# Kernel optimization log

Hardware: AMD Instinct MI355X
Metric: run time of the kernel (lower is better)

## Reference

```python
import jax, jax.numpy as jnp
import numpy as np

R = 4           # max_displacement
P = 2 * R + 1   # search_range = 9
DILATIONS = [[1], [1, 2, 3, 5, 9, 16]]
STRIDES = [4, 1]  # 8 // encoder_output_stride for strides [2, 8]
EPS = 1e-9


def _l2norm(x):
    # torch: x / (x.norm(dim=1, keepdim=True) + 1e-9)
    return x / (jnp.linalg.norm(x, axis=1, keepdims=True) + EPS)


def _corr(x1, x2, dilation, stride):
    """SpatialCorrelationSampler(patch_size=9, stride=stride, padding=0,
    dilation_patch=dilation): out[b,u,v,i,j] = sum_c x1[b,c,i*s,j*s] *
    x2[b,c,i*s+(u-R)*d, j*s+(v-R)*d], zero outside bounds."""
    B, C, H, W = x1.shape
    pad = R * dilation
    x2p = jnp.pad(x2, ((0, 0), (0, 0), (pad, pad), (pad, pad)))
    x1s = x1[:, :, ::stride, ::stride]  # (B,C,Ho,Wo)
    Ho, Wo = x1s.shape[2], x1s.shape[3]
    # all 81 (u,v) patch-offset slice starts in the padded map
    uv = jnp.stack(jnp.meshgrid(jnp.arange(P), jnp.arange(P), indexing='ij'),
                   axis=-1).reshape(-1, 2) * dilation  # (81, 2)

    def step(carry, start):
        x2uv = jax.lax.dynamic_slice(x2p, (0, 0, start[0], start[1]), (B, C, H, W))
        x2uv = x2uv[:, :, ::stride, ::stride]
        return carry, jnp.sum(x1s * x2uv, axis=1)  # (B,Ho,Wo)

    _, cost = jax.lax.scan(step, None, uv)  # (81,B,Ho,Wo)
    cost = cost.reshape(P, P, B, Ho, Wo)
    return jnp.transpose(cost, (2, 0, 1, 3, 4))  # (B,P,P,Ho,Wo)


def setup_inputs() -> dict:
    key = jax.random.key(0)
    k0, k1, k2, k3 = jax.random.split(key, 4)
    return {
        'x1_0': jax.random.normal(k0, (4, 256, 192, 256), dtype=jnp.float32),
        'x1_1': jax.random.normal(k1, (4, 256, 48, 64), dtype=jnp.float32),
        'x2_0': jax.random.normal(k2, (4, 256, 192, 256), dtype=jnp.float32),
        'x2_1': jax.random.normal(k3, (4, 256, 48, 64), dtype=jnp.float32),
    }


def reference(x1_0, x1_1, x2_0, x2_1):
    xs1, xs2 = [x1_0, x1_1], [x2_0, x2_1]
    cost_list = []
    for x1, x2, dils, s in zip(xs1, xs2, DILATIONS, STRIDES):
        x1n = _l2norm(x1)
        x2n = _l2norm(x2)
        per_dil = [_corr(x1n, x2n, d, s) for d in dils]  # each (B,P,P,Ho,Wo)
        # num_groups=1: per-dilation volumes stack into dim 1
        cost_list.append(jnp.stack(per_dil, axis=1))  # (B,nd,P,P,Ho,Wo)
    return jnp.concatenate(cost_list, axis=1)  # (B,7,9,9,48,64)
```

## Files before the change

### kernel.cpp

```cpp
#include <hip/hip_runtime.h>
#include <stdint.h>

#define EPSN 1e-9f

typedef __fp16 f16x8 __attribute__((ext_vector_type(8)));
typedef float f32x4 __attribute__((ext_vector_type(4)));

#define LDS_FENCE()                                        \
  do {                                                     \
    asm volatile("s_waitcnt lgkmcnt(0)" ::: "memory");     \
    __builtin_amdgcn_sched_barrier(0);                     \
  } while (0)


__global__ __launch_bounds__(256) void norms1_kernel(
    const float* __restrict__ x1_1, const float* __restrict__ x2_1,
    float* __restrict__ ws) {
  int p = blockIdx.x * 256 + threadIdx.x;
  const float* src = (p < 12288) ? x1_1 : x2_1;
  int q = (p < 12288) ? p : p - 12288;
  long base = (long)(q / 3072) * 786432 + (q % 3072);
  float ss = 0.f;
#pragma unroll 8
  for (int c = 0; c < 256; ++c) { float v = src[base + (long)c * 3072]; ss += v * v; }
  ws[p] = 1.f / (sqrtf(ss) + EPSN);
}

__global__ __launch_bounds__(256) void xpose0_kernel(
    const float* __restrict__ x1, __fp16* __restrict__ x1h0) {
  int bx = blockIdx.x;
  int i = bx % 48, b = bx / 48;
  __fp16* dst = x1h0 + (long)(b * 48 + i) * 16384;
  __shared__ uint32_t lds[64 * 128];
  __shared__ float sred[4][64];
  int t = threadIdx.x;
  int j = t & 63, cg = t >> 6;
  const float* sp = x1 + (long)b * 12582912 + (long)(4 * i) * 256 + 4 * j;
  float vv[64];
  float ss = 0.f;
#pragma unroll
  for (int c8 = 0; c8 < 64; ++c8) {
    float v = sp[(long)(cg * 64 + c8) * 49152];
    vv[c8] = v;
    ss += v * v;
  }
  sred[cg][j] = ss;
  __syncthreads();
  float invv = 1.f / (sqrtf(sred[0][j] + sred[1][j] + sred[2][j] + sred[3][j]) + EPSN);
#pragma unroll
  for (int cb = 0; cb < 8; ++cb) {
    uint32_t pk[4];
#pragma unroll
    for (int e2 = 0; e2 < 4; ++e2) {
      int cl = cb * 8 + e2 * 2;
      __fp16 h0 = (__fp16)(vv[cl] * invv);
      __fp16 h1 = (__fp16)(vv[cl + 1] * invv);
      pk[e2] = (uint32_t)__builtin_bit_cast(uint16_t, h0) |
               ((uint32_t)__builtin_bit_cast(uint16_t, h1) << 16);
    }
    int byteoff = j * 512 + ((cg * 128 + cb * 16) ^ ((j & 7) << 4));
    *reinterpret_cast<uint4*>(reinterpret_cast<char*>(lds) + byteoff) =
        make_uint4(pk[0], pk[1], pk[2], pk[3]);
  }
  __syncthreads();
#pragma unroll
  for (int rep = 0; rep < 8; ++rep) {
    int idx = rep * 256 + t;
    int jj = idx >> 5, cb = idx & 31;
    int byteoff = jj * 512 + ((cb * 16) ^ ((jj & 7) << 4));
    uint4 val = *reinterpret_cast<const uint4*>(
        reinterpret_cast<const char*>(lds) + byteoff);
    *reinterpret_cast<uint4*>(reinterpret_cast<char*>(dst) + jj * 512 + cb * 16) = val;
  }
}

__global__ __launch_bounds__(256) void corr0f_kernel(
    const __fp16* __restrict__ x1h, const float* __restrict__ x2,
    float* __restrict__ out) {
  int bx = blockIdx.x;
  int L = (bx & 7) * 96 + (bx >> 3);
  int y = L % 192, b = L / 192;
  int tid = threadIdx.x;
  int w = tid >> 6, lane = tid & 63;
  int i_lo = (y - 1) / 4; if (i_lo < 0) i_lo = 0;
  int i_hi = (y + 4) / 4; if (i_hi > 47) i_hi = 47;
  int NI = i_hi - i_lo + 1;

  __shared__ float red[4][31][64];
  __shared__ float inv2s[264];

  float acc[3][9];
#pragma unroll
  for (int r = 0; r < 3; ++r)
#pragma unroll
    for (int v = 0; v < 9; ++v) acc[r][v] = 0.f;
  float sq0 = 0.f, sq1 = 0.f, sq2 = 0.f, sq3 = 0.f;

  const float* x2row = x2 + (long)b * 12582912 + (long)y * 256 + 4 * lane;
  int lm = (lane == 0) ? 0 : lane - 1;
  int lp = (lane == 63) ? 63 : lane + 1;
  const __fp16 *pc[3], *pl[3], *pr[3];
#pragma unroll
  for (int r = 0; r < 3; ++r) {
    int ir = i_lo + r; if (ir > 47) ir = 47;
    const __fp16* base = x1h + (long)(b * 48 + ir) * 16384;
    pc[r] = base + lane * 256;
    pl[r] = base + lm * 256;
    pr[r] = base + lp * 256;
  }

#pragma unroll 1
  for (int g = 0; g < 8; ++g) {
    int c0 = w * 64 + g * 8;
    float4 fv[8];
#pragma unroll
    for (int e = 0; e < 8; ++e)
      fv[e] = *reinterpret_cast<const float4*>(x2row + (long)(c0 + e) * 49152);
    f16x8 hc[3], hl[3], hr[3];
#pragma unroll
    for (int r = 0; r < 3; ++r) {
      hc[r] = __builtin_bit_cast(f16x8, *reinterpret_cast<const uint4*>(pc[r] + c0));
      hl[r] = __builtin_bit_cast(f16x8, *reinterpret_cast<const uint4*>(pl[r] + c0));
      hr[r] = __builtin_bit_cast(f16x8, *reinterpret_cast<const uint4*>(pr[r] + c0));
    }
#pragma unroll
    for (int e = 0; e < 8; ++e) {
      float4 f = fv[e];
      sq0 += f.x * f.x; sq1 += f.y * f.y; sq2 += f.z * f.z; sq3 += f.w * f.w;
#pragma unroll
      for (int r = 0; r < 3; ++r) {
        float xv  = (float)hc[r][e];
        float xrr = (float)hr[r][e];
        float xll = (float)hl[r][e];
        acc[r][0] += xrr * f.x; acc[r][1] += xrr * f.y;
        acc[r][2] += xrr * f.z; acc[r][3] += xrr * f.w;
        acc[r][4] += xv * f.x;  acc[r][5] += xv * f.y;
        acc[r][6] += xv * f.z;  acc[r][7] += xv * f.w;
        acc[r][8] += xll * f.x;
      }
    }
  }

#pragma unroll
  for (int r = 0; r < 3; ++r) {
    acc[r][0] = __shfl_up(acc[r][0], 1);
    acc[r][1] = __shfl_up(acc[r][1], 1);
    acc[r][2] = __shfl_up(acc[r][2], 1);
    acc[r][3] = __shfl_up(acc[r][3], 1);
    acc[r][8] = __shfl_down(acc[r][8], 1);
  }

#pragma unroll
  for (int r = 0; r < 3; ++r)
#pragma unroll
    for (int v = 0; v < 9; ++v) red[w][r * 9 + v][lane] = acc[r][v];
  red[w][27][lane] = sq0; red[w][28][lane] = sq1;
  red[w][29][lane] = sq2; red[w][30][lane] = sq3;
  __syncthreads();
  {
    int comp = tid & 3, jj = tid >> 2;
    float ss = red[0][27 + comp][jj] + red[1][27 + comp][jj] +
               red[2][27 + comp][jj] + red[3][27 + comp][jj];
    inv2s[4 + tid] = 1.f / (sqrtf(ss) + EPSN);
    if (tid < 4) { inv2s[tid] = 0.f; inv2s[260 + tid] = 0.f; }
  }
  __syncthreads();
  int lim = NI * 576;
  for (int idx = tid; idx < lim; idx += 256) {
    int r = idx / 576, rem = idx - r * 576;
    int v = rem >> 6, j = rem & 63;
    int i_r = i_lo + r;
    int u_r = y - 4 * i_r + 4;
    float s = red[0][r * 9 + v][j] + red[1][r * 9 + v][j] +
              red[2][r * 9 + v][j] + red[3][r * 9 + v][j];
    out[(long)b * 1741824 + (long)u_r * 27648 + (long)v * 3072 + i_r * 64 + j] =
        s * inv2s[4 * j + v];
  }
}

__global__ __launch_bounds__(256) void corr0_fb_kernel(
    const float* __restrict__ x1b, const float* __restrict__ x2,
    float* __restrict__ out) {
  int bx = blockIdx.x;
  int L = (bx & 7) * 96 + (bx >> 3);
  int y = L % 192, b = L / 192;
  int tid = threadIdx.x;
  int w = tid >> 6, lane = tid & 63;
  int i_lo = (y - 1) / 4; if (i_lo < 0) i_lo = 0;
  int i_hi = (y + 4) / 4; if (i_hi > 47) i_hi = 47;
  int NI = i_hi - i_lo + 1;
  __shared__ float red[4][34][64];
  __shared__ float inv2s[264];
  __shared__ float inv1s[3][64];
  float acc[3][9];
#pragma unroll
  for (int r = 0; r < 3; ++r)
#pragma unroll
    for (int v = 0; v < 9; ++v) acc[r][v] = 0.f;
  float sq0 = 0.f, sq1 = 0.f, sq2 = 0.f, sq3 = 0.f;
  float s1[3] = {0.f, 0.f, 0.f};
  const float* x2row = x2 + (long)b * 12582912 + (long)y * 256 + 4 * lane;
  const float* x1p[3];
#pragma unroll
  for (int r = 0; r < 3; ++r) {
    int ir = i_lo + r; if (ir > 47) ir = 47;
    x1p[r] = x1b + (long)b * 12582912 + (long)ir * 1024 + (long)lane * 4;
  }
#pragma unroll 4
  for (int cc = 0; cc < 64; ++cc) {
    int c = w * 64 + cc;
    long off2 = (long)c * 49152;
    long off1 = (long)c * 49152;
    float4 f = *reinterpret_cast<const float4*>(x2row + off2);
    sq0 += f.x * f.x; sq1 += f.y * f.y; sq2 += f.z * f.z; sq3 += f.w * f.w;
#pragma unroll
    for (int r = 0; r < 3; ++r) {
      float xv = x1p[r][off1];
      float xr = __shfl_down(xv, 1);
      float xl = __shfl_up(xv, 1);
      s1[r] += xv * xv;
      acc[r][0] += xr * f.x; acc[r][1] += xr * f.y;
      acc[r][2] += xr * f.z; acc[r][3] += xr * f.w;
      acc[r][4] += xv * f.x; acc[r][5] += xv * f.y;
      acc[r][6] += xv * f.z; acc[r][7] += xv * f.w;
      acc[r][8] += xl * f.x;
    }
  }
#pragma unroll
  for (int r = 0; r < 3; ++r) {
    red[w][r * 9 + 0][lane] = __shfl_up(acc[r][0], 1);
    red[w][r * 9 + 1][lane] = __shfl_up(acc[r][1], 1);
    red[w][r * 9 + 2][lane] = __shfl_up(acc[r][2], 1);
    red[w][r * 9 + 3][lane] = __shfl_up(acc[r][3], 1);
    red[w][r * 9 + 4][lane] = acc[r][4];
    red[w][r * 9 + 5][lane] = acc[r][5];
    red[w][r * 9 + 6][lane] = acc[r][6];
    red[w][r * 9 + 7][lane] = acc[r][7];
    red[w][r * 9 + 8][lane] = __shfl_down(acc[r][8], 1);
    red[w][31 + r][lane] = s1[r];
  }
  red[w][27][lane] = sq0; red[w][28][lane] = sq1;
  red[w][29][lane] = sq2; red[w][30][lane] = sq3;
  __syncthreads();
  {
    int comp = tid & 3, jj = tid >> 2;
    float ss = red[0][27 + comp][jj] + red[1][27 + comp][jj] +
               red[2][27 + comp][jj] + red[3][27 + comp][jj];
    inv2s[4 + tid] = 1.f / (sqrtf(ss) + EPSN);
    if (tid < 4) { inv2s[tid] = 0.f; inv2s[260 + tid] = 0.f; }
    if (tid < 192) {
      int r = tid >> 6, j = tid & 63;
      float t = red[0][31 + r][j] + red[1][31 + r][j] +
                red[2][31 + r][j] + red[3][31 + r][j];
      inv1s[r][j] = 1.f / (sqrtf(t) + EPSN);
    }
  }
  __syncthreads();
  int lim = NI * 576;
  for (int idx = tid; idx < lim; idx += 256) {
    int r = idx / 576, rem = idx - r * 576;
    int v = rem >> 6, j = rem & 63;
    int i_r = i_lo + r;
    int u_r = y - 4 * i_r + 4;
    float s = red[0][r * 9 + v][j] + red[1][r * 9 + v][j] +
              red[2][r * 9 + v][j] + red[3][r * 9 + v][j];
    out[(long)b * 1741824 + (long)u_r * 27648 + (long)v * 3072 + i_r * 64 + j] =
        s * inv1s[r][j] * inv2s[4 * j + v];
  }
}

__global__ __launch_bounds__(256) void zfill0_kernel(float* __restrict__ out) {
  int idx = blockIdx.x * 256 + threadIdx.x;
  int b = idx / 2880, rem = idx - b * 2880;
  int k = rem / 576, rem2 = rem - k * 576;
  int v = rem2 >> 6, j = rem2 & 63;
  int u = (k < 4) ? k : 8;
  int i = (k < 4) ? 0 : 47;
  out[(long)b * 1741824 + (long)u * 27648 + (long)v * 3072 + i * 64 + j] = 0.f;
}

__global__ __launch_bounds__(256) void xpose1_kernel(
    const float* __restrict__ x1, const float* __restrict__ x2,
    __fp16* __restrict__ o1, __fp16* __restrict__ o2) {
  int bx = blockIdx.x;
  int tz = bx & 1; int rem = bx >> 1;
  int i = rem % 48, b = rem / 48;
  const float* src = tz ? x2 : x1;
  __fp16* dst = (tz ? o2 : o1) + (long)(b * 48 + i) * 16384;
  __shared__ uint32_t lds[64 * 128];
  __shared__ float sred[4][64];
  int t = threadIdx.x;
  int j = t & 63, cg = t >> 6;
  const float* sp = src + (long)b * 786432 + (long)i * 64 + j;
  float vv[64];
  float ss = 0.f;
#pragma unroll
  for (int c8 = 0; c8 < 64; ++c8) {
    float v = sp[(long)(cg * 64 + c8) * 3072];
    vv[c8] = v;
    ss += v * v;
  }
  sred[cg][j] = ss;
  __syncthreads();
  float invv = 1.f / (sqrtf(sred[0][j] + sred[1][j] + sred[2][j] + sred[3][j]) + EPSN);
#pragma unroll
  for (int cb = 0; cb < 8; ++cb) {
    uint32_t pk[4];
#pragma unroll
    for (int e2 = 0; e2 < 4; ++e2) {
      int cl = cb * 8 + e2 * 2;
      __fp16 h0 = (__fp16)(vv[cl] * invv);
      __fp16 h1 = (__fp16)(vv[cl + 1] * invv);
      pk[e2] = (uint32_t)__builtin_bit_cast(uint16_t, h0) |
               ((uint32_t)__builtin_bit_cast(uint16_t, h1) << 16);
    }
    int byteoff = j * 512 + ((cg * 128 + cb * 16) ^ ((j & 7) << 4));
    *reinterpret_cast<uint4*>(reinterpret_cast<char*>(lds) + byteoff) =
        make_uint4(pk[0], pk[1], pk[2], pk[3]);
  }
  __syncthreads();
#pragma unroll
  for (int rep = 0; rep < 8; ++rep) {
    int idx = rep * 256 + t;
    int jj = idx >> 5, cb = idx & 31;
    int byteoff = jj * 512 + ((cb * 16) ^ ((jj & 7) << 4));
    uint4 val = *reinterpret_cast<const uint4*>(
        reinterpret_cast<const char*>(lds) + byteoff);
    *reinterpret_cast<uint4*>(reinterpret_cast<char*>(dst) + jj * 512 + cb * 16) = val;
  }
}

__device__ const int OFFS39[39] = {
    0, 1, -1, 2, -2, 3, -3, 4, -4, 5, -5, 6, -6, 8, -8, 9, -9, 10, -10,
    12, -12, 15, -15, 16, -16, 18, -18, 20, -20, 27, -27, 32, -32, 36, -36,
    48, -48, 64, -64};

__global__ __launch_bounds__(64) void corr1m_kernel(
    const __fp16* __restrict__ w1, const __fp16* __restrict__ w2,
    float* __restrict__ out) {
  const int dils[6] = {1, 2, 3, 5, 9, 16};
  int bx = blockIdx.x;
  int L = (bx & 7) * 936 + (bx >> 3);
  int oi = L % 39, i = (L / 39) % 48, b = L / 1872;
  int o = OFFS39[oi];
  int y = i + o;
  bool valid = (y >= 0 && y < 48);
  int l = threadIdx.x;
  __shared__ float c_lds[64][65];

  if (valid) {
    int lm = l & 15, lk = l >> 4;
    const __fp16* A = w1 + (long)(b * 48 + i) * 16384;
    const __fp16* B = w2 + (long)(b * 48 + y) * 16384;
    f32x4 acc[4][4];
#pragma unroll
    for (int tm = 0; tm < 4; ++tm)
#pragma unroll
      for (int tn = 0; tn < 4; ++tn) acc[tm][tn] = (f32x4)0.f;

    for (int ks = 0; ks < 8; ++ks) {
      f16x8 af[4], bf[4];
      int ko = ks * 32 + lk * 8;
#pragma unroll
      for (int tm = 0; tm < 4; ++tm)
        af[tm] = __builtin_bit_cast(f16x8, *reinterpret_cast<const uint4*>(
                     A + (tm * 16 + lm) * 256 + ko));
#pragma unroll
      for (int tn = 0; tn < 4; ++tn)
        bf[tn] = __builtin_bit_cast(f16x8, *reinterpret_cast<const uint4*>(
                     B + (tn * 16 + lm) * 256 + ko));
#pragma unroll
      for (int tm = 0; tm < 4; ++tm)
#pragma unroll
        for (int tn = 0; tn < 4; ++tn)
          acc[tm][tn] = __builtin_amdgcn_mfma_f32_16x16x32_f16(
              af[tm], bf[tn], acc[tm][tn], 0, 0, 0);
    }
#pragma unroll
    for (int tm = 0; tm < 4; ++tm)
#pragma unroll
      for (int tn = 0; tn < 4; ++tn)
#pragma unroll
        for (int r = 0; r < 4; ++r)
          c_lds[tm * 16 + lk * 4 + r][tn * 16 + lm] = acc[tm][tn][r];
    LDS_FENCE();
  }

#pragma unroll
  for (int dI = 0; dI < 6; ++dI) {
    int d = dils[dI];
    if (o % d) continue;
    int ud = o / d;
    if (ud < -4 || ud > 4) continue;
    long ob = (long)b * 1741824 + (long)(1 + dI) * 248832 +
              (long)(ud + 4) * 27648 + (long)i * 64 + l;
#pragma unroll
    for (int v = 0; v < 9; ++v) {
      float val = 0.f;
      if (valid) {
        int j2 = l + (v - 4) * d;
        val = (j2 >= 0 && j2 < 64) ? c_lds[l][j2] : 0.f;
      }
      out[ob + (long)v * 3072] = val;
    }
  }
}

__global__ __launch_bounds__(64) void corr1_kernel(
    const float* __restrict__ x1, const float* __restrict__ x2,
    const float* __restrict__ ws, float* __restrict__ out) {
  int bx = blockIdx.x;
  int L = (bx & 7) * 1296 + (bx >> 3);
  int u = L % 9, dI = (L / 9) % 6, i = (L / 54) % 48, b = L / 2592;
  const int dils[6] = {1, 2, 3, 5, 9, 16};
  int d = dils[dI];
  int y = i + (u - 4) * d;
  int lane = threadIdx.x;
  long ob = (long)b * 1741824 + (long)(1 + dI) * 248832 + (long)u * 27648 +
            (long)i * 64 + lane;
  if (y < 0 || y >= 48) {
#pragma unroll
    for (int v = 0; v < 9; ++v) out[ob + v * 3072] = 0.f;
    return;
  }
  __shared__ uint4 x2t[192];
  x2t[lane] = make_uint4(0, 0, 0, 0);
  x2t[lane + 64] = make_uint4(0, 0, 0, 0);
  x2t[lane + 128] = make_uint4(0, 0, 0, 0);
  float acc[9];
#pragma unroll
  for (int v = 0; v < 9; ++v) acc[v] = 0.f;
  const float* x2row = x2 + (long)b * 786432 + (long)y * 64 + lane;
  const float* x1row = x1 + (long)b * 786432 + (long)i * 64 + lane;
#pragma unroll 1
  for (int cc8 = 0; cc8 < 32; ++cc8) {
    float x1v[8]; uint32_t xb[8];
#pragma unroll
    for (int cc = 0; cc < 8; ++cc) {
      long c = cc8 * 8 + cc;
      xb[cc] = __float_as_uint(x2row[c * 3072]) + 0x8000u;
      x1v[cc] = x1row[c * 3072];
    }
    uint4 pk;
    pk.x = (xb[0] >> 16) | (xb[1] & 0xffff0000u);
    pk.y = (xb[2] >> 16) | (xb[3] & 0xffff0000u);
    pk.z = (xb[4] >> 16) | (xb[5] & 0xffff0000u);
    pk.w = (xb[6] >> 16) | (xb[7] & 0xffff0000u);
    x2t[64 + lane] = pk;
    LDS_FENCE();
#pragma unroll
    for (int v = 0; v < 9; ++v) {
      uint4 q = x2t[64 + lane + (v - 4) * d];
      float s;
      s  = x1v[0] * __uint_as_float(q.x << 16);
      s += x1v[1] * __uint_as_float(q.x & 0xffff0000u);
      s += x1v[2] * __uint_as_float(q.y << 16);
      s += x1v[3] * __uint_as_float(q.y & 0xffff0000u);
      s += x1v[4] * __uint_as_float(q.z << 16);
      s += x1v[5] * __uint_as_float(q.z & 0xffff0000u);
      s += x1v[6] * __uint_as_float(q.w << 16);
      s += x1v[7] * __uint_as_float(q.w & 0xffff0000u);
      acc[v] += s;
    }
    LDS_FENCE();
  }
  const float* i1 = ws + b * 3072 + i * 64;
  const float* i2 = ws + 12288 + b * 3072 + y * 64;
  float inv1 = i1[lane];
#pragma unroll
  for (int v = 0; v < 9; ++v) {
    int col = lane + (v - 4) * d;
    float i2v = (col >= 0 && col < 64) ? i2[col] : 0.f;
    out[ob + v * 3072] = acc[v] * inv1 * i2v;
  }
}

extern "C" void kernel_launch(void* const* d_in, const int* in_sizes, int n_in,
                              void* d_out, int out_size, void* d_ws, size_t ws_size,
                              hipStream_t stream) {
  const float* x1_0 = (const float*)d_in[0];
  const float* x1_1 = (const float*)d_in[1];
  const float* x2_0 = (const float*)d_in[2];
  const float* x2_1 = (const float*)d_in[3];
  float* out = (float*)d_out;
  float* ws = (float*)d_ws;
  if (ws_size >= 18972672) {
    __fp16* x1h0 = (__fp16*)((char*)d_ws + 12681216);
    xpose0_kernel<<<192, 256, 0, stream>>>(x1_0, x1h0);
    corr0f_kernel<<<768, 256, 0, stream>>>(x1h0, x2_0, out);
  } else {
    corr0_fb_kernel<<<768, 256, 0, stream>>>(x1_0, x2_0, out);
  }
  zfill0_kernel<<<45, 256, 0, stream>>>(out);
  if (ws_size >= 12681216) {
    __fp16* w1h = (__fp16*)((char*)d_ws + 98304);
    __fp16* w2h = w1h + 3145728;
    xpose1_kernel<<<384, 256, 0, stream>>>(x1_1, x2_1, w1h, w2h);
    corr1m_kernel<<<7488, 64, 0, stream>>>(w1h, w2h, out);
  } else {
    norms1_kernel<<<96, 256, 0, stream>>>(x1_1, x2_1, ws);
    corr1_kernel<<<10368, 64, 0, stream>>>(x1_1, x2_1, ws, out);
  }
}
```

Before: 138.0 us.

## Convert stride-4 level correlation to fp16 MFMA with pre-normalized transposed x2

Adds a transpose kernel that L2-normalizes the full-resolution x2 map, converts it to fp16 in a channel-contiguous padded layout, and zero-fills the border columns. The scalar FMA correlation kernel for level 0 is replaced with a per-(b,i,u) wavefront kernel that computes a 64x80 tile of dot products with 16x16x32 fp16 MFMA and gathers the 9 diagonal offsets from LDS. This moves the main dot-product work onto matrix cores. In exchange it makes an extra full pass over x2_0, needs a much larger workspace, and computes many tile entries that are thrown away.

Measured after the change: 168.9 us. 1.22x slower.

```diff
diff --git a/kernel.cpp b/kernel.cpp
--- a/kernel.cpp
+++ b/kernel.cpp
@@ -74,108 +74,104 @@
   }
 }
 
-__global__ __launch_bounds__(256) void corr0f_kernel(
-    const __fp16* __restrict__ x1h, const float* __restrict__ x2,
+__global__ __launch_bounds__(256) void xpose2_kernel(
+    const float* __restrict__ x2, __fp16* __restrict__ x2h) {
+  int bx = blockIdx.x;
+  int q = bx & 3; int rem = bx >> 2;
+  int y = rem % 192, b = rem / 192;
+  char* rowb = (char*)x2h + (long)(b * 192 + y) * 276 * 512;
+  char* dst = rowb + (long)(4 + 64 * q) * 512;
+  __shared__ uint32_t lds[64 * 128];
+  __shared__ float sred[4][64];
+  int t = threadIdx.x;
+  int j = t & 63, cg = t >> 6;
+  const float* sp = x2 + (long)b * 12582912 + (long)y * 256 + 64 * q + j;
+  float vv[64];
+  float ss = 0.f;
+#pragma unroll
+  for (int c8 = 0; c8 < 64; ++c8) {
+    float v = sp[(long)(cg * 64 + c8) * 49152];
+    vv[c8] = v;
+    ss += v * v;
+  }
+  sred[cg][j] = ss;
+  __syncthreads();
+  float invv = 1.f / (sqrtf(sred[0][j] + sred[1][j] + sred[2][j] + sred[3][j]) + EPSN);
+#pragma unroll
+  for (int cb = 0; cb < 8; ++cb) {
+    uint32_t pk[4];
+#pragma unroll
+    for (int e2 = 0; e2 < 4; ++e2) {
+      int cl = cb * 8 + e2 * 2;
+      __fp16 h0 = (__fp16)(vv[cl] * invv);
+      __fp16 h1 = (__fp16)(vv[cl + 1] * invv);
+      pk[e2] = (uint32_t)__builtin_bit_cast(uint16_t, h0) |
+               ((uint32_t)__builtin_bit_cast(uint16_t, h1) << 16);
+    }
+    int byteoff = j * 512 + ((cg * 128 + cb * 16) ^ ((j & 7) << 4));
+    *reinterpret_cast<uint4*>(reinterpret_cast<char*>(lds) + byteoff) =
+        make_uint4(pk[0], pk[1], pk[2], pk[3]);
+  }
+  __syncthreads();
+#pragma unroll
+  for (int rep = 0; rep < 8; ++rep) {
+    int idx = rep * 256 + t;
+    int jj = idx >> 5, cb = idx & 31;
+    int byteoff = jj * 512 + ((cb * 16) ^ ((jj & 7) << 4));
+    uint4 val = *reinterpret_cast<const uint4*>(
+        reinterpret_cast<const char*>(lds) + byteoff);
+    *reinterpret_cast<uint4*>(dst + jj * 512 + cb * 16) = val;
+  }
+  uint4 z = make_uint4(0, 0, 0, 0);
+  if (q == 0 && t < 128)
+    *reinterpret_cast<uint4*>(rowb + t * 16) = z;
+  if (q == 3) {
+    *reinterpret_cast<uint4*>(rowb + 133120 + t * 16) = z;
+    *reinterpret_cast<uint4*>(rowb + 133120 + 4096 + t * 16) = z;
+  }
+}
+
+__global__ __launch_bounds__(64) void corr0m_kernel(
+    const __fp16* __restrict__ x1h, const __fp16* __restrict__ x2h,
     float* __restrict__ out) {
   int bx = blockIdx.x;
-  int L = (bx & 7) * 96 + (bx >> 3);
-  int y = L % 192, b = L / 192;
-  int tid = threadIdx.x;
-  int w = tid >> 6, lane = tid & 63;
-  int i_lo = (y - 1) / 4; if (i_lo < 0) i_lo = 0;
-  int i_hi = (y + 4) / 4; if (i_hi > 47) i_hi = 47;
-  int NI = i_hi - i_lo + 1;
-
-  __shared__ float red[4][31][64];
-  __shared__ float inv2s[264];
-
-  float acc[3][9];
-#pragma unroll
-  for (int r = 0; r < 3; ++r)
-#pragma unroll
-    for (int v = 0; v < 9; ++v) acc[r][v] = 0.f;
-  float sq0 = 0.f, sq1 = 0.f, sq2 = 0.f, sq3 = 0.f;
-
-  const float* x2row = x2 + (long)b * 12582912 + (long)y * 256 + 4 * lane;
-  int lm = (lane == 0) ? 0 : lane - 1;
-  int lp = (lane == 63) ? 63 : lane + 1;
-  const __fp16 *pc[3], *pl[3], *pr[3];
-#pragma unroll
-  for (int r = 0; r < 3; ++r) {
-    int ir = i_lo + r; if (ir > 47) ir = 47;
-    const __fp16* base = x1h + (long)(b * 48 + ir) * 16384;
-    pc[r] = base + lane * 256;
-    pl[r] = base + lm * 256;
-    pr[r] = base + lp * 256;
-  }
-
-#pragma unroll 1
-  for (int g = 0; g < 8; ++g) {
-    int c0 = w * 64 + g * 8;
-    float4 fv[8];
-#pragma unroll
-    for (int e = 0; e < 8; ++e)
-      fv[e] = *reinterpret_cast<const float4*>(x2row + (long)(c0 + e) * 49152);
-    f16x8 hc[3], hl[3], hr[3];
-#pragma unroll
-    for (int r = 0; r < 3; ++r) {
-      hc[r] = __builtin_bit_cast(f16x8, *reinterpret_cast<const uint4*>(pc[r] + c0));
-      hl[r] = __builtin_bit_cast(f16x8, *reinterpret_cast<const uint4*>(pl[r] + c0));
-      hr[r] = __builtin_bit_cast(f16x8, *reinterpret_cast<const uint4*>(pr[r] + c0));
-    }
-#pragma unroll
-    for (int e = 0; e < 8; ++e) {
-      float4 f = fv[e];
-      sq0 += f.x * f.x; sq1 += f.y * f.y; sq2 += f.z * f.z; sq3 += f.w * f.w;
-#pragma unroll
-      for (int r = 0; r < 3; ++r) {
-        float xv  = (float)hc[r][e];
-        float xrr = (float)hr[r][e];
-        float xll = (float)hl[r][e];
-        acc[r][0] += xrr * f.x; acc[r][1] += xrr * f.y;
-        acc[r][2] += xrr * f.z; acc[r][3] += xrr * f.w;
-        acc[r][4] += xv * f.x;  acc[r][5] += xv * f.y;
-        acc[r][6] += xv * f.z;  acc[r][7] += xv * f.w;
-        acc[r][8] += xll * f.x;
+  int L = (bx & 7) * 216 + (bx >> 3);
+  int u = L % 9, i = (L / 9) % 48, b = L / 432;
+  int y = 4 * i + u - 4;
+  if (y < 0 || y >= 192) return;
+  int l = threadIdx.x, lm = l & 15, lk = l >> 4;
+  const __fp16* A = x1h + (long)(b * 48 + i) * 16384;
+  const __fp16* B = x2h + (long)(b * 192 + y) * 70656;
+  __shared__ float c_lds[64][82];
+
+#pragma unroll
+  for (int jt = 0; jt < 4; ++jt) {
+    f32x4 acc[5];
+#pragma unroll
+    for (int n = 0; n < 5; ++n) acc[n] = (f32x4)0.f;
+    for (int ks = 0; ks < 8; ++ks) {
+      int ko = ks * 32 + lk * 8;
+      f16x8 af = __builtin_bit_cast(f16x8, *reinterpret_cast<const uint4*>(
+                     A + (jt * 16 + lm) * 256 + ko));
+#pragma unroll
+      for (int n = 0; n < 5; ++n) {
+        f16x8 bf = __builtin_bit_cast(f16x8, *reinterpret_cast<const uint4*>(
+                       B + (long)(jt * 64 + n * 16 + lm) * 256 + ko));
+        acc[n] = __builtin_amdgcn_mfma_f32_16x16x32_f16(af, bf, acc[n], 0, 0, 0);
       }
     }
-  }
-
-#pragma unroll
-  for (int r = 0; r < 3; ++r) {
-    acc[r][0] = __shfl_up(acc[r][0], 1);
-    acc[r][1] = __shfl_up(acc[r][1], 1);
-    acc[r][2] = __shfl_up(acc[r][2], 1);
-    acc[r][3] = __shfl_up(acc[r][3], 1);
-    acc[r][8] = __shfl_down(acc[r][8], 1);
-  }
-
-#pragma unroll
-  for (int r = 0; r < 3; ++r)
-#pragma unroll
-    for (int v = 0; v < 9; ++v) red[w][r * 9 + v][lane] = acc[r][v];
-  red[w][27][lane] = sq0; red[w][28][lane] = sq1;
-  red[w][29][lane] = sq2; red[w][30][lane] = sq3;
-  __syncthreads();
-  {
-    int comp = tid & 3, jj = tid >> 2;
-    float ss = red[0][27 + comp][jj] + red[1][27 + comp][jj] +
-               red[2][27 + comp][jj] + red[3][27 + comp][jj];
-    inv2s[4 + tid] = 1.f / (sqrtf(ss) + EPSN);
-    if (tid < 4) { inv2s[tid] = 0.f; inv2s[260 + tid] = 0.f; }
-  }
-  __syncthreads();
-  int lim = NI * 576;
-  for (int idx = tid; idx < lim; idx += 256) {
-    int r = idx / 576, rem = idx - r * 576;
-    int v = rem >> 6, j = rem & 63;
-    int i_r = i_lo + r;
-    int u_r = y - 4 * i_r + 4;
-    float s = red[0][r * 9 + v][j] + red[1][r * 9 + v][j] +
-              red[2][r * 9 + v][j] + red[3][r * 9 + v][j];
-    out[(long)b * 1741824 + (long)u_r * 27648 + (long)v * 3072 + i_r * 64 + j] =
-        s * inv2s[4 * j + v];
-  }
+#pragma unroll
+    for (int n = 0; n < 5; ++n)
+#pragma unroll
+      for (int r = 0; r < 4; ++r)
+        c_lds[jt * 16 + lk * 4 + r][n * 16 + lm] = acc[n][r];
+  }
+  LDS_FENCE();
+
+  long ob = (long)b * 1741824 + (long)u * 27648 + (long)i * 64 + l;
+#pragma unroll
+  for (int v = 0; v < 9; ++v)
+    out[ob + (long)v * 3072] = c_lds[l][4 * (l & 15) + v];
 }
 
 __global__ __launch_bounds__(256) void corr0_fb_kernel(
@@ -209,13 +205,12 @@
 #pragma unroll 4
   for (int cc = 0; cc < 64; ++cc) {
     int c = w * 64 + cc;
-    long off2 = (long)c * 49152;
-    long off1 = (long)c * 49152;
-    float4 f = *reinterpret_cast<const float4*>(x2row + off2);
+    long off = (long)c * 49152;
+    float4 f = *reinterpret_cast<const float4*>(x2row + off);
     sq0 += f.x * f.x; sq1 += f.y * f.y; sq2 += f.z * f.z; sq3 += f.w * f.w;
 #pragma unroll
     for (int r = 0; r < 3; ++r) {
-      float xv = x1p[r][off1];
+      float xv = x1p[r][off];
       float xr = __shfl_down(xv, 1);
       float xl = __shfl_up(xv, 1);
       s1[r] += xv * xv;
@@ -484,10 +479,12 @@
   const float* x2_1 = (const float*)d_in[3];
   float* out = (float*)d_out;
   float* ws = (float*)d_ws;
-  if (ws_size >= 18972672) {
+  if (ws_size >= 127500288) {
     __fp16* x1h0 = (__fp16*)((char*)d_ws + 12681216);
+    __fp16* x2h0 = (__fp16*)((char*)d_ws + 18972672);
     xpose0_kernel<<<192, 256, 0, stream>>>(x1_0, x1h0);
-    corr0f_kernel<<<768, 256, 0, stream>>>(x1h0, x2_0, out);
+    xpose2_kernel<<<3072, 256, 0, stream>>>(x2_0, x2h0);
+    corr0m_kernel<<<1728, 64, 0, stream>>>(x1h0, x2h0, out);
   } else {
     corr0_fb_kernel<<<768, 256, 0, stream>>>(x1_0, x2_0, out);
   }
```
